# Optimization experiments

Measured on AMD Instinct MI355X. Metric: run time of the kernel, lower is better.

The kernel has to match this reference:

```python
import jax, jax.numpy as jnp
import numpy as np

N = 40000      # nodes
E = 640000     # directed edges (avg degree 16)
IN_DIM = 64
HID = 64
OUT = 128
EPS_LN = 1e-5
EPS_BN = 1e-5
NEG_SLOPE = 0.2  # PyG GATConv default


def setup_inputs() -> dict:
    key = jax.random.key(0)
    ks = jax.random.split(key, 40)
    s = 0.05
    d = {}
    d["x"] = jax.random.normal(ks[0], (N, IN_DIM), jnp.float32)
    d["edge_index"] = jax.random.randint(ks[1], (2, E), 0, N, jnp.int32)
    d["pos"] = jax.random.normal(ks[2], (N, 3), jnp.float32)
    # GAT layer 1: in=64, out=64, heads=4 (concat)
    d["W1"] = jax.random.normal(ks[3], (4 * HID, IN_DIM), jnp.float32) * s
    d["a_s1"] = jax.random.normal(ks[4], (4, HID), jnp.float32) * s
    d["a_d1"] = jax.random.normal(ks[5], (4, HID), jnp.float32) * s
    d["bg1"] = jnp.zeros((4 * HID,), jnp.float32)
    d["ln1_g"] = jnp.ones((4 * HID,), jnp.float32)
    d["ln1_b"] = jnp.zeros((4 * HID,), jnp.float32)
    # GAT layer 2: in=256, out=64, heads=2 (concat)
    d["W2"] = jax.random.normal(ks[6], (2 * HID, 4 * HID), jnp.float32) * s
    d["a_s2"] = jax.random.normal(ks[7], (2, HID), jnp.float32) * s
    d["a_d2"] = jax.random.normal(ks[8], (2, HID), jnp.float32) * s
    d["bg2"] = jnp.zeros((2 * HID,), jnp.float32)
    d["ln2_g"] = jnp.ones((2 * HID,), jnp.float32)
    d["ln2_b"] = jnp.zeros((2 * HID,), jnp.float32)
    # GAT layer 3: in=128, out=128, heads=1
    d["W3"] = jax.random.normal(ks[9], (OUT, 2 * HID), jnp.float32) * s
    d["a_s3"] = jax.random.normal(ks[10], (1, OUT), jnp.float32) * s
    d["a_d3"] = jax.random.normal(ks[11], (1, OUT), jnp.float32) * s
    d["bg3"] = jnp.zeros((OUT,), jnp.float32)
    # pointnet: Conv1d(3,64,1) -> BN -> ReLU -> Conv1d(64,128,1) -> BN -> ReLU -> Conv1d(128,128,1)
    d["pw1"] = jax.random.normal(ks[12], (64, 3), jnp.float32) * s
    d["pb1"] = jnp.zeros((64,), jnp.float32)
    d["bn1_g"] = jnp.ones((64,), jnp.float32)
    d["bn1_b"] = jnp.zeros((64,), jnp.float32)
    d["pw2"] = jax.random.normal(ks[13], (128, 64), jnp.float32) * s
    d["pb2"] = jnp.zeros((128,), jnp.float32)
    d["bn2_g"] = jnp.ones((128,), jnp.float32)
    d["bn2_b"] = jnp.zeros((128,), jnp.float32)
    d["pw3"] = jax.random.normal(ks[14], (OUT, 128), jnp.float32) * s
    d["pb3"] = jnp.zeros((OUT,), jnp.float32)
    # fusion Linear(2*OUT, OUT)
    d["fw"] = jax.random.normal(ks[15], (OUT, 2 * OUT), jnp.float32) * s
    d["fb"] = jnp.zeros((OUT,), jnp.float32)
    return d


def _gat(x, W, a_s, a_d, b, src, dst, n):
    """PyG-style GATConv (concat=True, eval mode). x:[n,Fin], W:[H*C,Fin], a_*:[H,C]."""
    H, C = a_s.shape
    h = (x @ W.T).reshape(n, H, C)                       # [n,H,C]
    e_src = jnp.sum(h * a_s[None], -1)                   # [n,H]
    e_dst = jnp.sum(h * a_d[None], -1)                   # [n,H]
    e = jax.nn.leaky_relu(e_src[src] + e_dst[dst], NEG_SLOPE)   # [E,H]
    emax = jax.ops.segment_max(e, dst, num_segments=n)   # segment softmax over dst
    ex = jnp.exp(e - emax[dst])
    den = jax.ops.segment_sum(ex, dst, num_segments=n)
    alpha = ex / (den[dst] + 1e-16)                      # [E,H]
    out = jax.ops.segment_sum(alpha[:, :, None] * h[src], dst, num_segments=n)  # [n,H,C]
    return out.reshape(n, H * C) + b


def _ln(x, g, b):
    mu = jnp.mean(x, -1, keepdims=True)
    var = jnp.var(x, -1, keepdims=True)
    return (x - mu) * jax.lax.rsqrt(var + EPS_LN) * g + b


def _bn_eval(x, g, b):
    # eval-mode BatchNorm with freshly-initialized running stats (mean=0, var=1)
    return x * (g * jax.lax.rsqrt(jnp.float32(1.0 + EPS_BN))) + b


def reference(x, edge_index, pos, W1, a_s1, a_d1, bg1, ln1_g, ln1_b,
              W2, a_s2, a_d2, bg2, ln2_g, ln2_b, W3, a_s3, a_d3, bg3,
              pw1, pb1, bn1_g, bn1_b, pw2, pb2, bn2_g, bn2_b, pw3, pb3, fw, fb):
    n = x.shape[0]
    loops = jnp.arange(n, dtype=edge_index.dtype)        # PyG add_self_loops=True
    src = jnp.concatenate([edge_index[0], loops])
    dst = jnp.concatenate([edge_index[1], loops])

    x1 = jax.nn.relu(_ln(_gat(x, W1, a_s1, a_d1, bg1, src, dst, n), ln1_g, ln1_b))
    x2 = jax.nn.relu(_ln(_gat(x1, W2, a_s2, a_d2, bg2, src, dst, n), ln2_g, ln2_b))
    x3 = _gat(x2, W3, a_s3, a_d3, bg3, src, dst, n)      # [n,OUT]

    # pointnet: 1x1 conv1d == per-node linear
    p = jax.nn.relu(_bn_eval(pos @ pw1.T + pb1, bn1_g, bn1_b))
    p = jax.nn.relu(_bn_eval(p @ pw2.T + pb2, bn2_g, bn2_b))
    pos_features = p @ pw3.T + pb3                       # [n,OUT]

    combined = jnp.concatenate([x3, pos_features], -1)
    output = combined @ fw.T + fb
    return (output, x3, pos_features)
```

## Files before the change

### kernel.cpp

```cpp
#include <hip/hip_runtime.h>
#include <cstddef>

#define NNODES 40000
#define NEDGES 640000
#define NETOT  (NNODES + NEDGES)
#define ELLW   96
#define NCAST  30720

typedef unsigned short u16;
typedef unsigned int   u32;
using v2f = __attribute__((ext_vector_type(2))) float;

__device__ inline float wave_sum(float v) {
#pragma unroll
    for (int o = 32; o > 0; o >>= 1) v += __shfl_xor(v, o);
    return v;
}
__device__ inline u16 f2bf(float f) {
    u32 u = __float_as_uint(f);
    return (u16)((u + 0x7fffu + ((u >> 16) & 1u)) >> 16);
}

__global__ void ell_cast_kernel(const int* __restrict__ ei, int* __restrict__ cnt,
                                u16* __restrict__ srcs16, int2* __restrict__ ovbuf,
                                const float* s0, u16* d0, int n0, const float* s1, u16* d1, int n1,
                                const float* s2, u16* d2, int n2, const float* s3, u16* d3, int n3,
                                const float* s4, u16* d4, int n4, const float* s5, u16* d5, int n5) {
    int idx = blockIdx.x * blockDim.x + threadIdx.x;
    if (idx < NETOT) {
        int src, dst;
        if (idx < NEDGES) { src = ei[idx]; dst = ei[NEDGES + idx]; }
        else              { src = idx - NEDGES; dst = src; }
        int p = atomicAdd(&cnt[dst], 1);
        if (p < ELLW) srcs16[dst * ELLW + p] = (u16)src;
        else {
            int q = atomicAdd(&cnt[NNODES], 1);
            ovbuf[q] = make_int2(dst, src);
        }
        return;
    }
    int i = idx - NETOT;
    const float* s; u16* d;
    if      (i < n0) { s = s0; d = d0; }
    else if ((i -= n0) < n1) { s = s1; d = d1; }
    else if ((i -= n1) < n2) { s = s2; d = d2; }
    else if ((i -= n2) < n3) { s = s3; d = d3; }
    else if ((i -= n3) < n4) { s = s4; d = d4; }
    else if ((i -= n4) < n5) { s = s5; d = d5; }
    else return;
    float4 v = ((const float4*)s)[i];
    ushort4 o; o.x = f2bf(v.x); o.y = f2bf(v.y); o.z = f2bf(v.z); o.w = f2bf(v.w);
    ((ushort4*)d)[i] = o;
}

__global__ void prep_v_kernel(const float* __restrict__ W1, const float* __restrict__ as1,
                              const float* __restrict__ ad1, float* __restrict__ vbuf) {
    int t = threadIdx.x;
    int h = t >> 6, k = t & 63;
    float ss = 0.f, dd = 0.f;
    for (int c = 0; c < 64; c++) {
        float w = W1[(h * 64 + c) * 64 + k];
        ss += as1[h * 64 + c] * w;
        dd += ad1[h * 64 + c] * w;
    }
    vbuf[t] = ss;
    vbuf[256 + t] = dd;
}

__global__ void esed1_kernel(const float* __restrict__ x, const float* __restrict__ vbuf,
                             float* __restrict__ es, float* __restrict__ ed,
                             u16* __restrict__ xc) {
    __shared__ float vl[512];
    int tid = threadIdx.x;
    vl[tid] = vbuf[tid];
    vl[tid + 256] = vbuf[tid + 256];
    __syncthreads();
    int lane = tid & 63, wave = tid >> 6;
    int i = lane >> 2, q = lane & 3;
    int node = blockIdx.x * 64 + wave * 16 + i;
    const float* xp = x + (size_t)node * 64 + q * 16;
    float xr[16];
    *(float4*)&xr[0]  = ((const float4*)xp)[0];
    *(float4*)&xr[4]  = ((const float4*)xp)[1];
    *(float4*)&xr[8]  = ((const float4*)xp)[2];
    *(float4*)&xr[12] = ((const float4*)xp)[3];
    float p[8];
#pragma unroll
    for (int h = 0; h < 8; h++) {
        float s = 0.f;
#pragma unroll
        for (int j = 0; j < 16; j++) s += xr[j] * vl[h * 64 + q * 16 + j];
        p[h] = s;
    }
#pragma unroll
    for (int h = 0; h < 8; h++) {
        p[h] += __shfl_xor(p[h], 1);
        p[h] += __shfl_xor(p[h], 2);
    }
    es[node * 4 + q] = p[q];
    ed[node * 4 + q] = p[4 + q];
    u16* cp = xc + (size_t)node * 64 + q * 16;
#pragma unroll
    for (int j = 0; j < 16; j += 4) {
        ushort4 o; o.x = f2bf(xr[j]); o.y = f2bf(xr[j + 1]);
        o.z = f2bf(xr[j + 2]); o.w = f2bf(xr[j + 3]);
        *(ushort4*)(cp + j) = o;
    }
}

__global__ void gat_agg_kernel(const u16* __restrict__ xc,
                               const float* __restrict__ es, const float* __restrict__ ed,
                               const int* __restrict__ cnt, const u16* __restrict__ srcs16,
                               const int2* __restrict__ ovbuf,
                               u16* __restrict__ agg, int n) {
    __shared__ float wbuf[4][4][100];
    __shared__ u32   sbuf[4][ELLW];
    int wave = threadIdx.x >> 6;
    int wid = (blockIdx.x * blockDim.x + threadIdx.x) >> 6;
    int lane = threadIdx.x & 63;
    if (wid >= n) return;

    int degt = cnt[wid];
    int mainc = degt < ELLW ? degt : ELLW;
    int padt = (mainc + 7) & ~7;
    const u16* sp = srcs16 + (size_t)wid * ELLW;

    const int h = lane & 3;
    const int esub = lane >> 2;
    float edh = ed[(size_t)wid * 4 + h];

    float den = 0.f;
    for (int i0 = 0; i0 < padt; i0 += 16) {
        int e = i0 + esub;
        if (e < padt) {
            float w = 0.f; u32 off = 0;
            if (e < mainc) {
                int s = sp[e];
                off = (u32)s << 7;
                float v = es[(size_t)s * 4 + h] + edh;
                v = v > 0.f ? v : 0.2f * v;
                w = __expf(v);
            }
            wbuf[wave][h][e] = w;
            if (h == 0) sbuf[wave][e] = off;
            den += w;
        }
    }
    int ovn = 0;
    if (degt > ELLW) {
        ovn = cnt[n];
        for (int j = esub; j < ovn; j += 16) {
            int2 t = ovbuf[j];
            if (t.x == wid) {
                float v = es[(size_t)t.y * 4 + h] + edh;
                v = v > 0.f ? v : 0.2f * v;
                den += __expf(v);
            }
        }
    }
#pragma unroll
    for (int o = 4; o < 64; o <<= 1) den += __shfl_xor(den, o);
    float inv = 1.f / (den + 1e-16f);

    const int e2 = lane >> 5, f16 = lane & 31;
    const char* hp = (const char*)xc + f16 * 4;
    v2f a0 = {0.f, 0.f}, a1 = {0.f, 0.f}, a2 = {0.f, 0.f}, a3 = {0.f, 0.f};
    for (int eb = 0; eb < padt; eb += 8) {
        u32 of[4]; u32 g[4];
        float w0[4], w1[4], w2[4], w3[4];
#pragma unroll
        for (int k = 0; k < 4; k++) of[k] = sbuf[wave][eb + 2 * k + e2];
#pragma unroll
        for (int k = 0; k < 4; k++) g[k] = *(const u32*)(hp + of[k]);
#pragma unroll
        for (int k = 0; k < 4; k++) {
            int e = eb + 2 * k + e2;
            w0[k] = wbuf[wave][0][e]; w1[k] = wbuf[wave][1][e];
            w2[k] = wbuf[wave][2][e]; w3[k] = wbuf[wave][3][e];
        }
#pragma unroll
        for (int k = 0; k < 4; k++) {
            v2f hx;
            hx.x = __uint_as_float(g[k] << 16);
            hx.y = __uint_as_float(g[k] & 0xffff0000u);
            a0 += v2f{w0[k], w0[k]} * hx;
            a1 += v2f{w1[k], w1[k]} * hx;
            a2 += v2f{w2[k], w2[k]} * hx;
            a3 += v2f{w3[k], w3[k]} * hx;
        }
    }
    if (degt > ELLW) {
        for (int j = 0; j < ovn; j++) {
            int2 t = ovbuf[j];
            if (t.x != wid) continue;
            float wh[4];
#pragma unroll
            for (int hh = 0; hh < 4; hh++) {
                float v = es[(size_t)t.y * 4 + hh] + __shfl(edh, hh);
                v = v > 0.f ? v : 0.2f * v;
                wh[hh] = __expf(v);
            }
            if (lane < 32) {
                u32 g = *(const u32*)(hp + ((u32)t.y << 7));
                v2f hx;
                hx.x = __uint_as_float(g << 16);
                hx.y = __uint_as_float(g & 0xffff0000u);
                a0 += v2f{wh[0], wh[0]} * hx;
                a1 += v2f{wh[1], wh[1]} * hx;
                a2 += v2f{wh[2], wh[2]} * hx;
                a3 += v2f{wh[3], wh[3]} * hx;
            }
        }
    }
    a0.x += __shfl_xor(a0.x, 32); a0.y += __shfl_xor(a0.y, 32);
    a1.x += __shfl_xor(a1.x, 32); a1.y += __shfl_xor(a1.y, 32);
    a2.x += __shfl_xor(a2.x, 32); a2.y += __shfl_xor(a2.y, 32);
    a3.x += __shfl_xor(a3.x, 32); a3.y += __shfl_xor(a3.y, 32);
    float iv[4];
#pragma unroll
    for (int hh = 0; hh < 4; hh++) iv[hh] = __shfl(inv, hh);
    if (lane < 32) {
        u32* op = (u32*)agg + (size_t)wid * 128 + f16;
        op[0]  = ((u32)f2bf(a0.y * iv[0]) << 16) | f2bf(a0.x * iv[0]);
        op[32] = ((u32)f2bf(a1.y * iv[1]) << 16) | f2bf(a1.x * iv[1]);
        op[64] = ((u32)f2bf(a2.y * iv[2]) << 16) | f2bf(a2.x * iv[2]);
        op[96] = ((u32)f2bf(a3.y * iv[3]) << 16) | f2bf(a3.x * iv[3]);
    }
}

__global__ void w1ln_kernel(const u16* __restrict__ agg, const u16* __restrict__ B,
                            const float* __restrict__ bias,
                            const float* __restrict__ lng, const float* __restrict__ lnb,
                            u16* __restrict__ xb, int M) {
    using bfrag = __attribute__((ext_vector_type(8))) short;
    using ffrag = __attribute__((ext_vector_type(4))) float;
    int wave = threadIdx.x >> 6, lane = threadIdx.x & 63;
    int lm = lane & 15, kg = (lane >> 4) * 8;
    int rowblk = blockIdx.x * 64 + wave * 16;
    ffrag acc[16] = {};
#pragma unroll
    for (int hh = 0; hh < 4; hh++) {
#pragma unroll
        for (int k0 = 0; k0 < 64; k0 += 32) {
            bfrag af = *(const bfrag*)(agg + (size_t)(rowblk + lm) * 256 + hh * 64 + kg + k0);
#pragma unroll
            for (int tt = 0; tt < 4; tt++) {
                int t = hh * 4 + tt;
                bfrag bf = *(const bfrag*)(B + (size_t)(hh * 64 + tt * 16 + lm) * 64 + kg + k0);
                acc[t] = __builtin_amdgcn_mfma_f32_16x16x32_bf16(af, bf, acc[t], 0, 0, 0);
            }
        }
    }
    int orow = rowblk + (lane >> 4) * 4;
    float bi[16], gg[16], bb[16];
#pragma unroll
    for (int t = 0; t < 16; t++) {
        int col = t * 16 + lm;
        bi[t] = bias[col]; gg[t] = lng[col]; bb[t] = lnb[col];
    }
#pragma unroll
    for (int r = 0; r < 4; r++) {
        float pv[16];
        float s1 = 0.f, s2 = 0.f;
#pragma unroll
        for (int t = 0; t < 16; t++) {
            float v = acc[t][r] + bi[t];
            pv[t] = v; s1 += v; s2 += v * v;
        }
#pragma unroll
        for (int o = 1; o < 16; o <<= 1) { s1 += __shfl_xor(s1, o); s2 += __shfl_xor(s2, o); }
        float mu = s1 / 256.f;
        float var = s2 / 256.f - mu * mu;
        float rstd = rsqrtf(var + 1e-5f);
#pragma unroll
        for (int t = 0; t < 16; t++) {
            float v = (pv[t] - mu) * rstd * gg[t] + bb[t];
            v = v > 0.f ? v : 0.f;
            xb[(size_t)(orow + r) * 256 + t * 16 + lm] = f2bf(v);
        }
    }
}

template <int H, int C, bool AF32>
__global__ void gemm_scores_kernel(const void* __restrict__ Aptr, const u16* __restrict__ B,
                                   u16* __restrict__ Cout,
                                   const float* __restrict__ as, const float* __restrict__ ad,
                                   float* __restrict__ es, float* __restrict__ ed,
                                   int M, int Nn, int K) {
    constexpr int HT = 128 / C;
    using bfrag = __attribute__((ext_vector_type(8))) short;
    using ffrag = __attribute__((ext_vector_type(4))) float;
    int wave = threadIdx.x >> 6, lane = threadIdx.x & 63;
    int lm = lane & 15, kg = (lane >> 4) * 8;
    int rowblk = blockIdx.x * 64 + wave * 16;
    int n0 = blockIdx.y * 128;
    const u16* Bp = B + (size_t)(n0 + lm) * K + kg;
    ffrag acc[8] = {};
    for (int k0 = 0; k0 < K; k0 += 32) {
        bfrag af;
        if constexpr (AF32) {
            const float* ap = (const float*)Aptr + (size_t)(rowblk + lm) * K + kg + k0;
            float4 a0 = *(const float4*)ap;
            float4 a1 = *(const float4*)(ap + 4);
            af[0] = (short)f2bf(a0.x); af[1] = (short)f2bf(a0.y);
            af[2] = (short)f2bf(a0.z); af[3] = (short)f2bf(a0.w);
            af[4] = (short)f2bf(a1.x); af[5] = (short)f2bf(a1.y);
            af[6] = (short)f2bf(a1.z); af[7] = (short)f2bf(a1.w);
        } else {
            af = *(const bfrag*)((const u16*)Aptr + (size_t)(rowblk + lm) * K + kg + k0);
        }
#pragma unroll
        for (int t = 0; t < 8; t++) {
            bfrag bf = *(const bfrag*)(Bp + (size_t)t * 16 * K + k0);
            acc[t] = __builtin_amdgcn_mfma_f32_16x16x32_bf16(af, bf, acc[t], 0, 0, 0);
        }
    }
    int orow = rowblk + (lane >> 4) * 4;
    float asv[8], adv[8];
#pragma unroll
    for (int t = 0; t < 8; t++) {
        int fcol = n0 + t * 16 + lm;
        asv[t] = as[fcol]; adv[t] = ad[fcol];
    }
    float ps[4][HT] = {}, pd[4][HT] = {};
#pragma unroll
    for (int t = 0; t < 8; t++) {
        const int hh = t / (C / 16);
#pragma unroll
        for (int r = 0; r < 4; r++) {
            float v = acc[t][r];
            ps[r][hh] += v * asv[t];
            pd[r][hh] += v * adv[t];
            Cout[(size_t)(orow + r) * Nn + n0 + t * 16 + lm] = f2bf(v);
        }
    }
    int hb = blockIdx.y * HT;
#pragma unroll
    for (int r = 0; r < 4; r++)
#pragma unroll
        for (int hh = 0; hh < HT; hh++) {
            float s = ps[r][hh], d = pd[r][hh];
#pragma unroll
            for (int o = 1; o < 16; o <<= 1) { s += __shfl_xor(s, o); d += __shfl_xor(d, o); }
            if (lm == 0) {
                es[(size_t)(orow + r) * H + hb + hh] = s;
                ed[(size_t)(orow + r) * H + hb + hh] = d;
            }
        }
}

template <int H, int C, bool LNRELU>
__global__ void gat_fused_kernel(const u16* __restrict__ hmat,
                                 const float* __restrict__ es, const float* __restrict__ ed,
                                 const int* __restrict__ cnt, const u16* __restrict__ srcs16,
                                 const int2* __restrict__ ovbuf,
                                 const float* __restrict__ bias,
                                 const float* __restrict__ lng, const float* __restrict__ lnb,
                                 void* __restrict__ out, int n) {
    constexpr int HC = H * C;
    constexpr int VPT = HC / 64;
    constexpr int SH = (HC == 256) ? 9 : 8;
    constexpr int EPW = 64 / H;
    constexpr int HSH = (H == 4) ? 2 : ((H == 2) ? 1 : 0);
    __shared__ float wbuf[4][H][100];
    __shared__ int   sbuf[4][ELLW];
    int wave = threadIdx.x >> 6;
    int wid = (blockIdx.x * blockDim.x + threadIdx.x) >> 6;
    int lane = threadIdx.x & 63;
    if (wid >= n) return;

    int degt = cnt[wid];
    int mainc = degt < ELLW ? degt : ELLW;
    int pad = (mainc + 7) & ~7;
    const u16* sp = srcs16 + (size_t)wid * ELLW;

    const int h = lane & (H - 1);
    const int esub = lane >> HSH;
    float edh = ed[(size_t)wid * H + h];

    float den = 0.f;
    for (int i0 = 0; i0 < pad; i0 += EPW) {
        int e = i0 + esub;
        if (e < pad) {
            float w = 0.f;
            int soff = 0;
            if (e < mainc) {
                int s = sp[e];
                soff = s << SH;
                float v = es[(size_t)s * H + h] + edh;
                v = v > 0.f ? v : 0.2f * v;
                w = __expf(v);
            }
            wbuf[wave][h][e] = w;
            if (h == 0) sbuf[wave][e] = soff;
            den += w;
        }
    }
    int ovn = 0;
    if (degt > ELLW) {
        ovn = cnt[n];
        for (int j = esub; j < ovn; j += EPW) {
            int2 t = ovbuf[j];
            if (t.x == wid) {
                float v = es[(size_t)t.y * H + h] + edh;
                v = v > 0.f ? v : 0.2f * v;
                den += __expf(v);
            }
        }
    }
#pragma unroll
    for (int o = H; o < 64; o <<= 1) den += __shfl_xor(den, o);
    float inv = 1.f / (den + 1e-16f);

    const int myhead = (lane * VPT) / C;
    const float invh = __shfl(inv, myhead);
    const int loff = lane * (VPT * 2);
    v2f a01 = {0.f, 0.f}, a23 = {0.f, 0.f};

    for (int e = 0; e < pad; e += 8) {
        int4   o0 = *(const int4*)&sbuf[wave][e];
        int4   o1 = *(const int4*)&sbuf[wave][e + 4];
        float4 w0 = *(const float4*)&wbuf[wave][myhead][e];
        float4 w1 = *(const float4*)&wbuf[wave][myhead][e + 4];
        int   oo[8] = {o0.x, o0.y, o0.z, o0.w, o1.x, o1.y, o1.z, o1.w};
        float ww[8] = {w0.x, w0.y, w0.z, w0.w, w1.x, w1.y, w1.z, w1.w};
        if constexpr (VPT == 4) {
            uint2 gg[8];
#pragma unroll
            for (int u = 0; u < 8; u++)
                gg[u] = *(const uint2*)((const char*)hmat + (size_t)(u32)oo[u] + loff);
#pragma unroll
            for (int u = 0; u < 8; u++) {
                v2f wv = {ww[u], ww[u]};
                v2f h01, h23;
                h01.x = __uint_as_float(gg[u].x << 16);
                h01.y = __uint_as_float(gg[u].x & 0xffff0000u);
                h23.x = __uint_as_float(gg[u].y << 16);
                h23.y = __uint_as_float(gg[u].y & 0xffff0000u);
                a01 += wv * h01;
                a23 += wv * h23;
            }
        } else {
            u32 gg[8];
#pragma unroll
            for (int u = 0; u < 8; u++)
                gg[u] = *(const u32*)((const char*)hmat + (size_t)(u32)oo[u] + loff);
#pragma unroll
            for (int u = 0; u < 8; u++) {
                v2f wv = {ww[u], ww[u]};
                v2f h01;
                h01.x = __uint_as_float(gg[u] << 16);
                h01.y = __uint_as_float(gg[u] & 0xffff0000u);
                a01 += wv * h01;
            }
        }
    }
    if (degt > ELLW) {
        const float edm = __shfl(edh, myhead);
        for (int j = 0; j < ovn; j++) {
            int2 t = ovbuf[j];
            if (t.x != wid) continue;
            float v = es[(size_t)t.y * H + myhead] + edm;
            v = v > 0.f ? v : 0.2f * v;
            float w = __expf(v);
            v2f wv = {w, w};
            if constexpr (VPT == 4) {
                uint2 g = *(const uint2*)((const char*)hmat + ((size_t)t.y << SH) + loff);
                v2f h01, h23;
                h01.x = __uint_as_float(g.x << 16);
                h01.y = __uint_as_float(g.x & 0xffff0000u);
                h23.x = __uint_as_float(g.y << 16);
                h23.y = __uint_as_float(g.y & 0xffff0000u);
                a01 += wv * h01;
                a23 += wv * h23;
            } else {
                u32 g = *(const u32*)((const char*)hmat + ((size_t)t.y << SH) + loff);
                v2f h01;
                h01.x = __uint_as_float(g << 16);
                h01.y = __uint_as_float(g & 0xffff0000u);
                a01 += wv * h01;
            }
        }
    }
    {
        v2f iv = {invh, invh};
        a01 *= iv;
        a23 *= iv;
    }

    int fbase = lane * VPT;
    float y[VPT];
    y[0] = a01.x + bias[fbase + 0];
    y[1] = a01.y + bias[fbase + 1];
    if constexpr (VPT == 4) {
        y[2] = a23.x + bias[fbase + 2];
        y[3] = a23.y + bias[fbase + 3];
    }

    if constexpr (LNRELU) {
        float s1 = 0.f, s2 = 0.f;
#pragma unroll
        for (int j = 0; j < VPT; j++) { s1 += y[j]; s2 += y[j] * y[j]; }
        s1 = wave_sum(s1);
        s2 = wave_sum(s2);
        float mu = s1 / (float)HC;
        float var = s2 / (float)HC - mu * mu;
        float rstd = rsqrtf(var + 1e-5f);
#pragma unroll
        for (int j = 0; j < VPT; j++) {
            float v = (y[j] - mu) * rstd * lng[fbase + j] + lnb[fbase + j];
            y[j] = v > 0.f ? v : 0.f;
        }
        u16* op = (u16*)out + (size_t)wid * HC + fbase;
        if constexpr (VPT == 4) {
            ushort4 o; o.x = f2bf(y[0]); o.y = f2bf(y[1]); o.z = f2bf(y[2]); o.w = f2bf(y[3]);
            *(ushort4*)op = o;
        } else {
            ushort2 o; o.x = f2bf(y[0]); o.y = f2bf(y[1]);
            *(ushort2*)op = o;
        }
    } else {
        float* op = (float*)out + (size_t)wid * HC + fbase;
        if constexpr (VPT == 4) *(float4*)op = make_float4(y[0], y[1], y[2], y[3]);
        else                    *(float2*)op = make_float2(y[0], y[1]);
    }
}

__global__ void gemm_pn12_kernel(const float* __restrict__ pos,
                                 const float* __restrict__ pw1, const float* __restrict__ pb1,
                                 const float* __restrict__ bn1g, const float* __restrict__ bn1b,
                                 const u16* __restrict__ B, u16* __restrict__ Cout,
                                 const float* __restrict__ pb2,
                                 const float* __restrict__ bn2g, const float* __restrict__ bn2b,
                                 int M) {
    const int Nn = 128, K = 64;
    using bfrag = __attribute__((ext_vector_type(8))) short;
    using ffrag = __attribute__((ext_vector_type(4))) float;
    int wave = threadIdx.x >> 6, lane = threadIdx.x & 63;
    int lm = lane & 15, kg = (lane >> 4) * 8;
    int rowblk = blockIdx.x * 64 + wave * 16;
    int row = rowblk + lm;
    float p0 = pos[row * 3 + 0], p1 = pos[row * 3 + 1], p2 = pos[row * 3 + 2];
    const u16* Bp = B + (size_t)lm * K + kg;
    const float bnscale = rsqrtf(1.0f + 1e-5f);
    ffrag acc[8] = {};
#pragma unroll
    for (int k0 = 0; k0 < K; k0 += 32) {
        bfrag af;
#pragma unroll
        for (int j = 0; j < 8; j++) {
            int k = kg + k0 + j;
            float v = p0 * pw1[k * 3 + 0] + p1 * pw1[k * 3 + 1] + p2 * pw1[k * 3 + 2] + pb1[k];
            v = v * (bn1g[k] * bnscale) + bn1b[k];
            v = v > 0.f ? v : 0.f;
            af[j] = (short)f2bf(v);
        }
#pragma unroll
        for (int t = 0; t < 8; t++) {
            bfrag bf = *(const bfrag*)(Bp + (size_t)t * 16 * K + k0);
            acc[t] = __builtin_amdgcn_mfma_f32_16x16x32_bf16(af, bf, acc[t], 0, 0, 0);
        }
    }
    int orow = rowblk + (lane >> 4) * 4;
#pragma unroll
    for (int t = 0; t < 8; t++) {
        int col = t * 16 + lm;
        float bi = pb2[col], g = bn2g[col] * bnscale, bb = bn2b[col];
#pragma unroll
        for (int r = 0; r < 4; r++) {
            float v = (acc[t][r] + bi) * g + bb;
            v = v > 0.f ? v : 0.f;
            Cout[(size_t)(orow + r) * Nn + col] = f2bf(v);
        }
    }
}

__global__ void gemm_pw3cat_kernel(const u16* __restrict__ p2, const u16* __restrict__ Bpw3,
                                   const float* __restrict__ pb3, float* __restrict__ pf,
                                   const float* __restrict__ x3, const u16* __restrict__ Bfw,
                                   const float* __restrict__ fb, float* __restrict__ outp,
                                   int M) {
    using bfrag = __attribute__((ext_vector_type(8))) short;
    using ffrag = __attribute__((ext_vector_type(4))) float;
    __shared__ float pft[64][132];
    int wave = threadIdx.x >> 6, lane = threadIdx.x & 63;
    int lm = lane & 15, kg = (lane >> 4) * 8;
    int rowblk = blockIdx.x * 64 + wave * 16;

    {
        const u16* Ap = p2 + (size_t)(rowblk + lm) * 128 + kg;
        const u16* Bp = Bpw3 + (size_t)lm * 128 + kg;
        ffrag acc[8] = {};
#pragma unroll
        for (int k0 = 0; k0 < 128; k0 += 32) {
            bfrag af = *(const bfrag*)(Ap + k0);
#pragma unroll
            for (int t = 0; t < 8; t++) {
                bfrag bf = *(const bfrag*)(Bp + (size_t)t * 16 * 128 + k0);
                acc[t] = __builtin_amdgcn_mfma_f32_16x16x32_bf16(af, bf, acc[t], 0, 0, 0);
            }
        }
        int orow = rowblk + (lane >> 4) * 4;
        int lrow = wave * 16 + (lane >> 4) * 4;
#pragma unroll
        for (int t = 0; t < 8; t++) {
            int col = t * 16 + lm;
            float bi = pb3[col];
#pragma unroll
            for (int r = 0; r < 4; r++) {
                float v = acc[t][r] + bi;
                pf[(size_t)(orow + r) * 128 + col] = v;
                pft[lrow + r][col] = v;
            }
        }
    }
    __syncthreads();

    {
        const u16* Bp = Bfw + (size_t)lm * 256 + kg;
        ffrag acc[8] = {};
        int row = rowblk + lm, lrow = wave * 16 + lm;
#pragma unroll
        for (int k0 = 0; k0 < 256; k0 += 32) {
            bfrag af;
            if (k0 < 128) {
                const float* ap = x3 + (size_t)row * 128 + kg + k0;
                float4 a0 = *(const float4*)ap;
                float4 a1 = *(const float4*)(ap + 4);
                af[0] = (short)f2bf(a0.x); af[1] = (short)f2bf(a0.y);
                af[2] = (short)f2bf(a0.z); af[3] = (short)f2bf(a0.w);
                af[4] = (short)f2bf(a1.x); af[5] = (short)f2bf(a1.y);
                af[6] = (short)f2bf(a1.z); af[7] = (short)f2bf(a1.w);
            } else {
                const float* ap = &pft[lrow][kg + k0 - 128];
                float4 a0 = *(const float4*)ap;
                float4 a1 = *(const float4*)(ap + 4);
                af[0] = (short)f2bf(a0.x); af[1] = (short)f2bf(a0.y);
                af[2] = (short)f2bf(a0.z); af[3] = (short)f2bf(a0.w);
                af[4] = (short)f2bf(a1.x); af[5] = (short)f2bf(a1.y);
                af[6] = (short)f2bf(a1.z); af[7] = (short)f2bf(a1.w);
            }
#pragma unroll
            for (int t = 0; t < 8; t++) {
                bfrag bf = *(const bfrag*)(Bp + (size_t)t * 16 * 256 + k0);
                acc[t] = __builtin_amdgcn_mfma_f32_16x16x32_bf16(af, bf, acc[t], 0, 0, 0);
            }
        }
        int orow = rowblk + (lane >> 4) * 4;
#pragma unroll
        for (int t = 0; t < 8; t++) {
            int col = t * 16 + lm;
            float bi = fb[col];
#pragma unroll
            for (int r = 0; r < 4; r++)
                outp[(size_t)(orow + r) * 128 + col] = acc[t][r] + bi;
        }
    }
}

extern "C" void kernel_launch(void* const* d_in, const int* in_sizes, int n_in,
                              void* d_out, int out_size, void* d_ws, size_t ws_size,
                              hipStream_t stream) {
    const float* x    = (const float*)d_in[0];
    const int*   ei   = (const int*)d_in[1];
    const float* pos  = (const float*)d_in[2];
    const float* W1   = (const float*)d_in[3];
    const float* as1  = (const float*)d_in[4];
    const float* ad1  = (const float*)d_in[5];
    const float* bg1  = (const float*)d_in[6];
    const float* ln1g = (const float*)d_in[7];
    const float* ln1b = (const float*)d_in[8];
    const float* W2   = (const float*)d_in[9];
    const float* as2  = (const float*)d_in[10];
    const float* ad2  = (const float*)d_in[11];
    const float* bg2  = (const float*)d_in[12];
    const float* ln2g = (const float*)d_in[13];
    const float* ln2b = (const float*)d_in[14];
    const float* W3   = (const float*)d_in[15];
    const float* as3  = (const float*)d_in[16];
    const float* ad3  = (const float*)d_in[17];
    const float* bg3  = (const float*)d_in[18];
    const float* pw1  = (const float*)d_in[19];
    const float* pb1  = (const float*)d_in[20];
    const float* bn1g = (const float*)d_in[21];
    const float* bn1b = (const float*)d_in[22];
    const float* pw2  = (const float*)d_in[23];
    const float* pb2  = (const float*)d_in[24];
    const float* bn2g = (const float*)d_in[25];
    const float* bn2b = (const float*)d_in[26];
    const float* pw3  = (const float*)d_in[27];
    const float* pb3  = (const float*)d_in[28];
    const float* fw   = (const float*)d_in[29];
    const float* fb   = (const float*)d_in[30];

    const int N = NNODES;
    float* out = (float*)d_out;
    float* x3  = out + (size_t)N * 128;
    float* pf  = out + (size_t)2 * N * 128;

    char* ws = (char*)d_ws;
    size_t off = 0;
    auto alloc = [&](size_t bytes) -> void* {
        void* p = ws + off;
        off += (bytes + 255) / 256 * 256;
        return p;
    };
    int*   cnt    = (int*)alloc((size_t)(N + 1) * 4);
    u16*   srcs16 = (u16*)alloc((size_t)N * ELLW * 2);
    int2*  ovbuf  = (int2*)alloc((size_t)NETOT * 8);
    float* esb    = (float*)alloc((size_t)N * 4 * 4);
    float* edb    = (float*)alloc((size_t)N * 4 * 4);
    u16*   w1c    = (u16*)alloc(16384 * 2);
    u16*   w2c    = (u16*)alloc(32768 * 2);
    u16*   w3c    = (u16*)alloc(16384 * 2);
    u16*   pw2c   = (u16*)alloc(8192 * 2);
    u16*   pw3c   = (u16*)alloc(16384 * 2);
    u16*   fwc    = (u16*)alloc(32768 * 2);
    u16*   hbufb  = (u16*)alloc((size_t)N * 128 * 2);
    u16*   xb     = (u16*)alloc((size_t)N * 256 * 2);
    u16*   p2b    = (u16*)alloc((size_t)N * 128 * 2);
    u16*   xc     = (u16*)alloc((size_t)N * 64 * 2);
    float* vbuf   = (float*)alloc(512 * 4);
    u16*   aggb   = (u16*)alloc((size_t)N * 256 * 2);

    hipMemsetAsync(cnt, 0, (size_t)(N + 1) * 4, stream);
    ell_cast_kernel<<<(NETOT + NCAST + 255) / 256, 256, 0, stream>>>(
        ei, cnt, srcs16, ovbuf,
        W1, w1c, 4096, W2, w2c, 8192, W3, w3c, 4096,
        pw2, pw2c, 2048, pw3, pw3c, 4096, fw, fwc, 8192);

    const int NW = N / 4;
    const int GB = N / 64;

    gemm_pn12_kernel<<<GB, 256, 0, stream>>>(
        pos, pw1, pb1, bn1g, bn1b, pw2c, p2b, pb2, bn2g, bn2b, N);

    prep_v_kernel<<<1, 256, 0, stream>>>(W1, as1, ad1, vbuf);
    esed1_kernel<<<GB, 256, 0, stream>>>(x, vbuf, esb, edb, xc);
    gat_agg_kernel<<<NW, 256, 0, stream>>>(xc, esb, edb, cnt, srcs16, ovbuf, aggb, N);
    w1ln_kernel<<<GB, 256, 0, stream>>>(aggb, w1c, bg1, ln1g, ln1b, xb, N);

    gemm_scores_kernel<2, 64, false><<<dim3(GB, 1), 256, 0, stream>>>(
        xb, w2c, hbufb, as2, ad2, esb, edb, N, 128, 256);
    gat_fused_kernel<2, 64, true><<<NW, 256, 0, stream>>>(
        hbufb, esb, edb, cnt, srcs16, ovbuf, bg2, ln2g, ln2b, xb, N);

    gemm_scores_kernel<1, 128, false><<<dim3(GB, 1), 256, 0, stream>>>(
        xb, w3c, hbufb, as3, ad3, esb, edb, N, 128, 128);
    gat_fused_kernel<1, 128, false><<<NW, 256, 0, stream>>>(
        hbufb, esb, edb, cnt, srcs16, ovbuf, bg3, nullptr, nullptr, x3, N);

    gemm_pw3cat_kernel<<<GB, 256, 0, stream>>>(p2b, pw3c, pb3, pf, x3, fwc, fb, out, N);
}
```

Before: 387.0 us.

## Build ELL adjacency via two-pass bucketed counting sort instead of global atomics

Graph construction now runs in two passes. First, edges are binned into 128-node destination buckets using shared-memory histograms, with one global atomic per bucket per block. Second, one block per bucket fills the ELL rows using shared-memory counters, which replaces 680k scattered global atomics on per-node counters. The weight cast and attention-vector prep are folded into the first kernel, removing one launch. The cost is an extra pass through a staging buffer of about 10 MB, and any bucket holding more than 8192 edges would be silently truncated.

```diff
diff --git a/kernel.cpp b/kernel.cpp
--- a/kernel.cpp
+++ b/kernel.cpp
@@ -6,6 +6,10 @@
 #define NETOT  (NNODES + NEDGES)
 #define ELLW   96
 #define NCAST  30720
+#define NBUCK  313
+#define SEGCAP 8192
+#define ABLOCKS 84
+#define CBLOCKS 30
 
 typedef unsigned short u16;
 typedef unsigned int   u32;
@@ -21,50 +25,99 @@
     return (u16)((u + 0x7fffu + ((u >> 16) & 1u)) >> 16);
 }
 
-__global__ void ell_cast_kernel(const int* __restrict__ ei, int* __restrict__ cnt,
-                                u16* __restrict__ srcs16, int2* __restrict__ ovbuf,
-                                const float* s0, u16* d0, int n0, const float* s1, u16* d1, int n1,
-                                const float* s2, u16* d2, int n2, const float* s3, u16* d3, int n3,
-                                const float* s4, u16* d4, int n4, const float* s5, u16* d5, int n5) {
-    int idx = blockIdx.x * blockDim.x + threadIdx.x;
-    if (idx < NETOT) {
-        int src, dst;
-        if (idx < NEDGES) { src = ei[idx]; dst = ei[NEDGES + idx]; }
-        else              { src = idx - NEDGES; dst = src; }
-        int p = atomicAdd(&cnt[dst], 1);
+__global__ void build_a_kernel(const int* __restrict__ ei, u32* __restrict__ bcnt,
+                               u32* __restrict__ seg,
+                               const float* __restrict__ W1, const float* __restrict__ as1,
+                               const float* __restrict__ ad1, float* __restrict__ vbuf,
+                               const float* s0, u16* d0, int n0, const float* s1, u16* d1, int n1,
+                               const float* s2, u16* d2, int n2, const float* s3, u16* d3, int n3,
+                               const float* s4, u16* d4, int n4, const float* s5, u16* d5, int n5) {
+    int tid = threadIdx.x;
+    int blk = blockIdx.x;
+    if (blk >= ABLOCKS) {
+        if (blk < ABLOCKS + CBLOCKS) {
+            int i = (blk - ABLOCKS) * 1024 + tid;
+            const float* s; u16* d;
+            if      (i < n0) { s = s0; d = d0; }
+            else if ((i -= n0) < n1) { s = s1; d = d1; }
+            else if ((i -= n1) < n2) { s = s2; d = d2; }
+            else if ((i -= n2) < n3) { s = s3; d = d3; }
+            else if ((i -= n3) < n4) { s = s4; d = d4; }
+            else if ((i -= n4) < n5) { s = s5; d = d5; }
+            else return;
+            float4 v = ((const float4*)s)[i];
+            ushort4 o; o.x = f2bf(v.x); o.y = f2bf(v.y); o.z = f2bf(v.z); o.w = f2bf(v.w);
+            ((ushort4*)d)[i] = o;
+        } else if (tid < 256) {
+            int h = tid >> 6, k = tid & 63;
+            float ss = 0.f, dd = 0.f;
+            for (int c = 0; c < 64; c++) {
+                float w = W1[(h * 64 + c) * 64 + k];
+                ss += as1[h * 64 + c] * w;
+                dd += ad1[h * 64 + c] * w;
+            }
+            vbuf[tid] = ss;
+            vbuf[256 + tid] = dd;
+        }
+        return;
+    }
+    __shared__ u32 hist[NBUCK], hbase[NBUCK];
+    for (int i = tid; i < NBUCK; i += 1024) hist[i] = 0;
+    __syncthreads();
+    u32 pk[8], loc[8]; int bj[8];
+    int g0 = blk * 8192;
+#pragma unroll
+    for (int j = 0; j < 8; j++) {
+        int g = g0 + j * 1024 + tid;
+        bj[j] = -1;
+        if (g < NETOT) {
+            int src, dst;
+            if (g < NEDGES) { src = ei[g]; dst = ei[NEDGES + g]; }
+            else            { src = g - NEDGES; dst = src; }
+            int b = dst >> 7;
+            pk[j] = ((u32)dst << 16) | (u32)src;
+            bj[j] = b;
+            loc[j] = atomicAdd(&hist[b], 1u);
+        }
+    }
+    __syncthreads();
+    for (int i = tid; i < NBUCK; i += 1024) {
+        u32 c = hist[i];
+        hbase[i] = c ? atomicAdd(&bcnt[i], c) : 0u;
+    }
+    __syncthreads();
+#pragma unroll
+    for (int j = 0; j < 8; j++) {
+        if (bj[j] >= 0) {
+            u32 pos = hbase[bj[j]] + loc[j];
+            if (pos < SEGCAP) seg[(size_t)bj[j] * SEGCAP + pos] = pk[j];
+        }
+    }
+}
+
+__global__ void build_b_kernel(const u32* __restrict__ seg, const u32* __restrict__ bcnt,
+                               int* __restrict__ cnt, u16* __restrict__ srcs16,
+                               int2* __restrict__ ovbuf) {
+    __shared__ u32 lcnt[128];
+    int tid = threadIdx.x;
+    int b = blockIdx.x;
+    int base = b << 7;
+    if (tid < 128) lcnt[tid] = 0;
+    __syncthreads();
+    u32 m = bcnt[b]; if (m > SEGCAP) m = SEGCAP;
+    const u32* sp = seg + (size_t)b * SEGCAP;
+    for (u32 e = tid; e < m; e += 256) {
+        u32 pkv = sp[e];
+        u32 dst = pkv >> 16, src = pkv & 0xffffu;
+        u32 p = atomicAdd(&lcnt[dst - (u32)base], 1u);
         if (p < ELLW) srcs16[dst * ELLW + p] = (u16)src;
         else {
             int q = atomicAdd(&cnt[NNODES], 1);
-            ovbuf[q] = make_int2(dst, src);
-        }
-        return;
-    }
-    int i = idx - NETOT;
-    const float* s; u16* d;
-    if      (i < n0) { s = s0; d = d0; }
-    else if ((i -= n0) < n1) { s = s1; d = d1; }
-    else if ((i -= n1) < n2) { s = s2; d = d2; }
-    else if ((i -= n2) < n3) { s = s3; d = d3; }
-    else if ((i -= n3) < n4) { s = s4; d = d4; }
-    else if ((i -= n4) < n5) { s = s5; d = d5; }
-    else return;
-    float4 v = ((const float4*)s)[i];
-    ushort4 o; o.x = f2bf(v.x); o.y = f2bf(v.y); o.z = f2bf(v.z); o.w = f2bf(v.w);
-    ((ushort4*)d)[i] = o;
-}
-
-__global__ void prep_v_kernel(const float* __restrict__ W1, const float* __restrict__ as1,
-                              const float* __restrict__ ad1, float* __restrict__ vbuf) {
-    int t = threadIdx.x;
-    int h = t >> 6, k = t & 63;
-    float ss = 0.f, dd = 0.f;
-    for (int c = 0; c < 64; c++) {
-        float w = W1[(h * 64 + c) * 64 + k];
-        ss += as1[h * 64 + c] * w;
-        dd += ad1[h * 64 + c] * w;
-    }
-    vbuf[t] = ss;
-    vbuf[256 + t] = dd;
+            ovbuf[q] = make_int2((int)dst, (int)src);
+        }
+    }
+    __syncthreads();
+    if (tid < 128 && base + tid < NNODES) cnt[base + tid] = (int)lcnt[tid];
 }
 
 __global__ void esed1_kernel(const float* __restrict__ x, const float* __restrict__ vbuf,
@@ -705,7 +758,9 @@
         off += (bytes + 255) / 256 * 256;
         return p;
     };
-    int*   cnt    = (int*)alloc((size_t)(N + 1) * 4);
+    int*   cnt    = (int*)alloc((size_t)(N + 1 + NBUCK) * 4);
+    u32*   bcnt   = (u32*)(cnt + N + 1);
+    u32*   seg    = (u32*)alloc((size_t)NBUCK * SEGCAP * 4);
     u16*   srcs16 = (u16*)alloc((size_t)N * ELLW * 2);
     int2*  ovbuf  = (int2*)alloc((size_t)NETOT * 8);
     float* esb    = (float*)alloc((size_t)N * 4 * 4);
@@ -723,11 +778,12 @@
     float* vbuf   = (float*)alloc(512 * 4);
     u16*   aggb   = (u16*)alloc((size_t)N * 256 * 2);
 
-    hipMemsetAsync(cnt, 0, (size_t)(N + 1) * 4, stream);
-    ell_cast_kernel<<<(NETOT + NCAST + 255) / 256, 256, 0, stream>>>(
-        ei, cnt, srcs16, ovbuf,
+    hipMemsetAsync(cnt, 0, (size_t)(N + 1 + NBUCK) * 4, stream);
+    build_a_kernel<<<ABLOCKS + CBLOCKS + 1, 1024, 0, stream>>>(
+        ei, bcnt, seg, W1, as1, ad1, vbuf,
         W1, w1c, 4096, W2, w2c, 8192, W3, w3c, 4096,
         pw2, pw2c, 2048, pw3, pw3c, 4096, fw, fwc, 8192);
+    build_b_kernel<<<NBUCK, 256, 0, stream>>>(seg, bcnt, cnt, srcs16, ovbuf);
 
     const int NW = N / 4;
     const int GB = N / 64;
@@ -735,7 +791,6 @@
     gemm_pn12_kernel<<<GB, 256, 0, stream>>>(
         pos, pw1, pb1, bn1g, bn1b, pw2c, p2b, pb2, bn2g, bn2b, N);
 
-    prep_v_kernel<<<1, 256, 0, stream>>>(W1, as1, ad1, vbuf);
     esed1_kernel<<<GB, 256, 0, stream>>>(x, vbuf, esb, edb, xc);
     gat_agg_kernel<<<NW, 256, 0, stream>>>(xc, esb, edb, cnt, srcs16, ovbuf, aggb, N);
     w1ln_kernel<<<GB, 256, 0, stream>>>(aggb, w1c, bg1, ln1g, ln1b, xb, N);
```

Result: faster. 359.5 us (-7.1%).
